# Kernel tuning notes

Measured on AMD Instinct MI355X. Metric: run time of the kernel, lower is better.

Reference implementation:

```python
import jax, jax.numpy as jnp
import numpy as np

BS, T = 128, 256
N_AGENTS, STATE_DIM, EMBED_DIM, HYPERNET_EMBED = 32, 512, 64, 256


def setup_inputs() -> dict:
    key = jax.random.key(0)
    ks = jax.random.split(key, 16)
    s = 0.02  # param init scale
    return {
        "agent_qs": jax.random.normal(ks[0], (BS, T, N_AGENTS), jnp.float32),
        "states": jax.random.normal(ks[1], (BS, T, STATE_DIM), jnp.float32),
        "w1_0": jax.random.normal(ks[2], (HYPERNET_EMBED, STATE_DIM), jnp.float32) * s,
        "b1_0": jax.random.normal(ks[3], (HYPERNET_EMBED,), jnp.float32) * s,
        "w1_2": jax.random.normal(ks[4], (EMBED_DIM * N_AGENTS, HYPERNET_EMBED), jnp.float32) * s,
        "b1_2": jax.random.normal(ks[5], (EMBED_DIM * N_AGENTS,), jnp.float32) * s,
        "wf_0": jax.random.normal(ks[6], (HYPERNET_EMBED, STATE_DIM), jnp.float32) * s,
        "bf_0": jax.random.normal(ks[7], (HYPERNET_EMBED,), jnp.float32) * s,
        "wf_2": jax.random.normal(ks[8], (EMBED_DIM, HYPERNET_EMBED), jnp.float32) * s,
        "bf_2": jax.random.normal(ks[9], (EMBED_DIM,), jnp.float32) * s,
        "hb_w": jax.random.normal(ks[10], (EMBED_DIM, STATE_DIM), jnp.float32) * s,
        "hb_b": jax.random.normal(ks[11], (EMBED_DIM,), jnp.float32) * s,
        "v0_w": jax.random.normal(ks[12], (EMBED_DIM, STATE_DIM), jnp.float32) * s,
        "v0_b": jax.random.normal(ks[13], (EMBED_DIM,), jnp.float32) * s,
        "v2_w": jax.random.normal(ks[14], (1, EMBED_DIM), jnp.float32) * s,
        "v2_b": jax.random.normal(ks[15], (1,), jnp.float32) * s,
    }


def reference(agent_qs, states, w1_0, b1_0, w1_2, b1_2, wf_0, bf_0, wf_2, bf_2,
              hb_w, hb_b, v0_w, v0_b, v2_w, v2_b):
    bs = agent_qs.shape[0]
    s = states.reshape(-1, STATE_DIM)          # [B, S]
    q = agent_qs.reshape(-1, 1, N_AGENTS)       # [B, 1, A]
    # hypernet-generated first-layer weights (positive via abs)
    h1 = jax.nn.relu(s @ w1_0.T + b1_0)
    w1 = jnp.abs(h1 @ w1_2.T + b1_2).reshape(-1, N_AGENTS, EMBED_DIM)  # [B, A, E]
    b1 = (s @ hb_w.T + hb_b).reshape(-1, 1, EMBED_DIM)                 # [B, 1, E]
    hidden = jax.nn.elu(jnp.einsum('bia,bae->bie', q, w1) + b1)        # [B, 1, E]
    # hypernet-generated final weights
    hf = jax.nn.relu(s @ wf_0.T + bf_0)
    w_final = jnp.abs(hf @ wf_2.T + bf_2).reshape(-1, EMBED_DIM, 1)    # [B, E, 1]
    v = (jax.nn.relu(s @ v0_w.T + v0_b) @ v2_w.T + v2_b).reshape(-1, 1, 1)
    y = jnp.einsum('bie,beo->bio', hidden, w_final) + v                # [B, 1, 1]
    return y.reshape(bs, -1, 1)
```

## Files before the change

### kernel.cpp

```cpp
#include <hip/hip_runtime.h>


#define SDIM 512
#define HD   256
#define EDIM 64
#define NAG  32

typedef short short8v __attribute__((ext_vector_type(8)));
typedef short short4v __attribute__((ext_vector_type(4)));
typedef float f32x4  __attribute__((ext_vector_type(4)));

__device__ __forceinline__ unsigned short f2bf(float f) {
  unsigned int u = __float_as_uint(f);
  unsigned int r = (u + 0x7FFFu + ((u >> 16) & 1u)) >> 16;
  return (unsigned short)r;
}
__device__ __forceinline__ float bf2f(unsigned short u) {
  return __uint_as_float(((unsigned int)u) << 16);
}
__device__ __forceinline__ short4v cvt4(float4 a) {
  short4v r;
  r[0] = (short)f2bf(a.x); r[1] = (short)f2bf(a.y);
  r[2] = (short)f2bf(a.z); r[3] = (short)f2bf(a.w);
  return r;
}

__global__ void qmix_convert(const float* __restrict__ w1_0, const float* __restrict__ wf_0,
                             const float* __restrict__ hb_w, const float* __restrict__ v0_w,
                             const float* __restrict__ w1_2, const float* __restrict__ wf_2,
                             unsigned short* __restrict__ W0cat, unsigned short* __restrict__ w12b,
                             unsigned short* __restrict__ wf2b) {
  int i = blockIdx.x * 256 + threadIdx.x;
  if (i < 327680) {
    float v;
    if (i < 131072)      v = w1_0[i];
    else if (i < 262144) v = wf_0[i - 131072];
    else if (i < 294912) v = hb_w[i - 262144];
    else                 v = v0_w[i - 294912];
    W0cat[i] = f2bf(v);
  } else if (i < 851968) {
    w12b[i - 327680] = f2bf(w1_2[i - 327680]);
  } else if (i < 868352) {
    wf2b[i - 851968] = f2bf(wf_2[i - 851968]);
  }
}

__global__ __launch_bounds__(512, 2) void qmix_k1(
    const float* __restrict__ states, const unsigned short* __restrict__ W0cat,
    const unsigned short* __restrict__ wf2b,
    const float* __restrict__ b1_0, const float* __restrict__ bf_0,
    const float* __restrict__ hb_b, const float* __restrict__ v0_b,
    const float* __restrict__ v2_w, const float* __restrict__ bf_2,
    unsigned short* __restrict__ h1g, unsigned short* __restrict__ b1h,
    unsigned short* __restrict__ wfinh, float* __restrict__ vbuf)
{
  __shared__ unsigned short sA[64 * 512];

  const int t    = threadIdx.x;
  const int r0   = blockIdx.x * 64;
  const int wave = t >> 6, lane = t & 63;
  const int lrow = lane & 15, lk = lane >> 4;

  const float4* gS4 = (const float4*)(states + (size_t)r0 * SDIM);
  float4 L[16];
#pragma unroll
  for (int it = 0; it < 16; it++) L[it] = gS4[it * 512 + t];

  const int colbase = wave * 80;
  const unsigned short* bp[5];
#pragma unroll
  for (int f = 0; f < 5; f++)
    bp[f] = W0cat + (size_t)(colbase + f * 16 + lrow) * SDIM + 8 * lk;
  short8v bregs[2][5];
#pragma unroll
  for (int f = 0; f < 5; f++) bregs[0][f] = *(const short8v*)(bp[f]);
#pragma unroll
  for (int f = 0; f < 5; f++) bregs[1][f] = *(const short8v*)(bp[f] + 32);

#pragma unroll
  for (int it = 0; it < 16; it++) {
    int idx = it * 512 + t;
    int row = idx >> 7, c4 = idx & 127;
    int byte = (row * 1024 + c4 * 8) ^ ((row & 7) << 4);
    *(short4v*)((char*)sA + byte) = cvt4(L[it]);
  }
  __syncthreads();

  f32x4 acc[4][5];
#pragma unroll
  for (int i = 0; i < 4; i++)
#pragma unroll
    for (int f = 0; f < 5; f++) acc[i][f] = (f32x4){0.f, 0.f, 0.f, 0.f};

#pragma unroll
  for (int ks = 0; ks < 16; ks++) {
    const int p = ks & 1;
    short8v af[4];
#pragma unroll
    for (int i = 0; i < 4; i++) {
      int row = i * 16 + lrow;
      int byte = (row * 1024 + ks * 64 + lk * 16) ^ ((row & 7) << 4);
      af[i] = *(const short8v*)((const char*)sA + byte);
    }
#pragma unroll
    for (int f = 0; f < 5; f++)
#pragma unroll
      for (int i = 0; i < 4; i++)
        acc[i][f] = __builtin_amdgcn_mfma_f32_16x16x32_bf16(af[i], bregs[p][f], acc[i][f], 0, 0, 0);
    if (ks < 14) {
#pragma unroll
      for (int f = 0; f < 5; f++) bregs[p][f] = *(const short8v*)(bp[f] + (ks + 2) * 32);
    }
  }

  __syncthreads();

  {
    float vs[4][4];
#pragma unroll
    for (int i = 0; i < 4; i++)
#pragma unroll
      for (int rr = 0; rr < 4; rr++) vs[i][rr] = 0.f;

#pragma unroll
    for (int f = 0; f < 5; f++) {
      int cb  = colbase + f * 16;
      int col = cb + lrow;
      if (cb < 512) {
        float bv = (cb < 256) ? b1_0[col] : bf_0[col - 256];
#pragma unroll
        for (int i = 0; i < 4; i++)
#pragma unroll
          for (int rr = 0; rr < 4; rr++) {
            int row = i * 16 + lk * 4 + rr;
            float v = fmaxf(acc[i][f][rr] + bv, 0.f);
            int byte = (row * 1024 + col * 2) ^ ((row & 7) << 4);
            *(unsigned short*)((char*)sA + byte) = f2bf(v);
          }
      } else if (cb < 576) {
        int e = col - 512;
        float bv = hb_b[e];
#pragma unroll
        for (int i = 0; i < 4; i++)
#pragma unroll
          for (int rr = 0; rr < 4; rr++) {
            int row = i * 16 + lk * 4 + rr;
            b1h[(size_t)(r0 + row) * EDIM + e] = f2bf(acc[i][f][rr] + bv);
          }
      } else {
        int e = col - 576;
        float bv = v0_b[e], wv = v2_w[e];
#pragma unroll
        for (int i = 0; i < 4; i++)
#pragma unroll
          for (int rr = 0; rr < 4; rr++)
            vs[i][rr] = fmaf(fmaxf(acc[i][f][rr] + bv, 0.f), wv, vs[i][rr]);
      }
    }
    if (colbase == 560) {
#pragma unroll
      for (int i = 0; i < 4; i++)
#pragma unroll
        for (int rr = 0; rr < 4; rr++) {
          float v = vs[i][rr];
#pragma unroll
          for (int m = 1; m < 16; m <<= 1) v += __shfl_xor(v, m, 64);
          if (lrow == 0) vbuf[r0 + i * 16 + lk * 4 + rr] = v;
        }
    }
  }
  __syncthreads();

  {
    const int wr2 = wave >> 1;
    const int wc2 = wave & 1;
    f32x4 wfa[2];
    wfa[0] = (f32x4){0.f, 0.f, 0.f, 0.f};
    wfa[1] = (f32x4){0.f, 0.f, 0.f, 0.f};
    const int row = wr2 * 16 + lrow;
#pragma unroll
    for (int kf = 0; kf < 8; kf++) {
      int byte = (row * 1024 + 512 + kf * 64 + lk * 16) ^ ((row & 7) << 4);
      short8v af2 = *(const short8v*)((const char*)sA + byte);
#pragma unroll
      for (int j = 0; j < 2; j++) {
        short8v bf2v = *(const short8v*)(wf2b + (size_t)(wc2 * 32 + j * 16 + lrow) * HD + kf * 32 + 8 * lk);
        wfa[j] = __builtin_amdgcn_mfma_f32_16x16x32_bf16(af2, bf2v, wfa[j], 0, 0, 0);
      }
    }
#pragma unroll
    for (int j = 0; j < 2; j++) {
      int e = wc2 * 32 + j * 16 + lrow;
#pragma unroll
      for (int r = 0; r < 4; r++) {
        int row2 = wr2 * 16 + lk * 4 + r;
        wfinh[(size_t)(r0 + row2) * EDIM + e] = f2bf(fabsf(wfa[j][r] + bf_2[e]));
      }
    }
  }

  {
    char* dst = (char*)h1g + (size_t)r0 * 512;
#pragma unroll
    for (int u = 0; u < 4; u++) {
      int idx = u * 512 + t;
      int row = idx >> 5;
      int p   = (idx & 31) * 16;
      short8v v = *(const short8v*)((const char*)sA + row * 1024 + p);
      *(short8v*)(dst + row * 512 + p) = v;
    }
  }
}

__global__ __launch_bounds__(512, 1) void qmix_k2(
    const unsigned short* __restrict__ h1g, const unsigned short* __restrict__ w12b,
    const float* __restrict__ agent_qs, const float* __restrict__ b1_2,
    const unsigned short* __restrict__ b1h, const unsigned short* __restrict__ wfinh,
    const float* __restrict__ vbuf, const float* __restrict__ v2_b,
    float* __restrict__ out)
{
  __shared__ unsigned char h1s[128 * 512];
  __shared__ unsigned short bbuf[2][16384];
  __shared__ float q_t[NAG * 136];
  __shared__ float ypart[2][128];

  const int t    = threadIdx.x;
  const int r0   = blockIdx.x * 128;
  const int wave = t >> 6, lane = t & 63;
  const int lrow = lane & 15, lk = lane >> 4;
  const int wr = wave >> 1;
  const int wc = wave & 1;

  short8v Lh[8];
  {
    const char* src = (const char*)h1g + (size_t)r0 * 512;
#pragma unroll
    for (int it = 0; it < 8; it++)
      Lh[it] = *(const short8v*)(src + (it * 512 + t) * 16);
  }
  const float4* gq = (const float4*)(agent_qs + (size_t)r0 * NAG);
  float4 q0 = gq[t], q1 = gq[512 + t];
  short8v sreg[4];
#pragma unroll
  for (int rd = 0; rd < 4; rd++)
    sreg[rd] = *(const short8v*)(w12b + rd * 4096 + t * 8);

  {
#pragma unroll
    for (int it = 0; it < 8; it++)
      *(short8v*)(h1s + (it * 512 + t) * 16) = Lh[it];
    int row0 = t >> 3, a4 = (t & 7) * 4;
    q_t[(a4 + 0) * 136 + row0] = q0.x;
    q_t[(a4 + 1) * 136 + row0] = q0.y;
    q_t[(a4 + 2) * 136 + row0] = q0.z;
    q_t[(a4 + 3) * 136 + row0] = q0.w;
    int row1 = 64 + row0;
    q_t[(a4 + 0) * 136 + row1] = q1.x;
    q_t[(a4 + 1) * 136 + row1] = q1.y;
    q_t[(a4 + 2) * 136 + row1] = q1.z;
    q_t[(a4 + 3) * 136 + row1] = q1.w;
#pragma unroll
    for (int rd = 0; rd < 4; rd++) {
      int Lo = rd * 8192 + t * 16;
      *(short8v*)((char*)bbuf + (Lo ^ (((Lo >> 9) & 7) << 4))) = sreg[rd];
    }
  }
  __syncthreads();

  short8v afr[2][8];
#pragma unroll
  for (int i = 0; i < 2; i++) {
    int row = wr * 32 + i * 16 + lrow;
#pragma unroll
    for (int kf = 0; kf < 8; kf++)
      afr[i][kf] = *(const short8v*)(h1s + row * 512 + ((kf * 64 + lk * 16) ^ ((row & 7) << 4)));
  }

  f32x4 hac00 = (f32x4){0.f,0.f,0.f,0.f}, hac01 = (f32x4){0.f,0.f,0.f,0.f};
  f32x4 hac10 = (f32x4){0.f,0.f,0.f,0.f}, hac11 = (f32x4){0.f,0.f,0.f,0.f};

#pragma unroll 1
  for (int a = 0; a < NAG; a++) {
    if (a < NAG - 1) {
      const unsigned short* p = w12b + (size_t)(a + 1) * 16384;
#pragma unroll
      for (int rd = 0; rd < 4; rd++)
        sreg[rd] = *(const short8v*)(p + rd * 4096 + t * 8);
    }
    const char* rbase = (const char*)bbuf + (a & 1) * 32768;

    f32x4 T00 = (f32x4){0.f,0.f,0.f,0.f}, T01 = (f32x4){0.f,0.f,0.f,0.f};
    f32x4 T10 = (f32x4){0.f,0.f,0.f,0.f}, T11 = (f32x4){0.f,0.f,0.f,0.f};
    const int e0 = wc * 32 + lrow, e1 = e0 + 16;
#pragma unroll
    for (int kf = 0; kf < 8; kf++) {
      short8v b0  = *(const short8v*)(rbase + ((e0 * 512 + kf * 64 + lk * 16) ^ ((e0 & 7) << 4)));
      short8v b1v = *(const short8v*)(rbase + ((e1 * 512 + kf * 64 + lk * 16) ^ ((e1 & 7) << 4)));
      T00 = __builtin_amdgcn_mfma_f32_16x16x32_bf16(afr[0][kf], b0,  T00, 0, 0, 0);
      T10 = __builtin_amdgcn_mfma_f32_16x16x32_bf16(afr[1][kf], b0,  T10, 0, 0, 0);
      T01 = __builtin_amdgcn_mfma_f32_16x16x32_bf16(afr[0][kf], b1v, T01, 0, 0, 0);
      T11 = __builtin_amdgcn_mfma_f32_16x16x32_bf16(afr[1][kf], b1v, T11, 0, 0, 0);
    }
    float bb0 = b1_2[a * EDIM + e0];
    float bb1 = b1_2[a * EDIM + e1];
    float4 qa = *(const float4*)(&q_t[a * 136 + wr * 32 + lk * 4]);
    float4 qb = *(const float4*)(&q_t[a * 136 + wr * 32 + 16 + lk * 4]);
#pragma unroll
    for (int r = 0; r < 4; r++) {
      float qar = (r == 0) ? qa.x : (r == 1) ? qa.y : (r == 2) ? qa.z : qa.w;
      float qbr = (r == 0) ? qb.x : (r == 1) ? qb.y : (r == 2) ? qb.z : qb.w;
      hac00[r] = fmaf(qar, fabsf(T00[r] + bb0), hac00[r]);
      hac01[r] = fmaf(qar, fabsf(T01[r] + bb1), hac01[r]);
      hac10[r] = fmaf(qbr, fabsf(T10[r] + bb0), hac10[r]);
      hac11[r] = fmaf(qbr, fabsf(T11[r] + bb1), hac11[r]);
    }
    if (a < NAG - 1) {
      char* wb = (char*)bbuf + ((a & 1) ^ 1) * 32768;
#pragma unroll
      for (int rd = 0; rd < 4; rd++) {
        int Lo = rd * 8192 + t * 16;
        *(short8v*)(wb + (Lo ^ (((Lo >> 9) & 7) << 4))) = sreg[rd];
      }
    }
    __syncthreads();
  }

  {
    float ys0[4], ys1[4];
    const int e0 = wc * 32 + lrow, e1 = e0 + 16;
#pragma unroll
    for (int r = 0; r < 4; r++) {
      int row0 = wr * 32 + lk * 4 + r;
      int row1 = row0 + 16;
      size_t g0 = (size_t)(r0 + row0) * EDIM;
      size_t g1 = (size_t)(r0 + row1) * EDIM;
      float p00 = hac00[r] + bf2f(b1h[g0 + e0]);
      float p01 = hac01[r] + bf2f(b1h[g0 + e1]);
      float p10 = hac10[r] + bf2f(b1h[g1 + e0]);
      float p11 = hac11[r] + bf2f(b1h[g1 + e1]);
      float h00 = p00 > 0.f ? p00 : expm1f(p00);
      float h01 = p01 > 0.f ? p01 : expm1f(p01);
      float h10 = p10 > 0.f ? p10 : expm1f(p10);
      float h11 = p11 > 0.f ? p11 : expm1f(p11);
      ys0[r] = h00 * bf2f(wfinh[g0 + e0]) + h01 * bf2f(wfinh[g0 + e1]);
      ys1[r] = h10 * bf2f(wfinh[g1 + e0]) + h11 * bf2f(wfinh[g1 + e1]);
    }
#pragma unroll
    for (int m = 1; m < 16; m <<= 1)
#pragma unroll
      for (int r = 0; r < 4; r++) {
        ys0[r] += __shfl_xor(ys0[r], m, 64);
        ys1[r] += __shfl_xor(ys1[r], m, 64);
      }
    if (lrow == 0) {
#pragma unroll
      for (int r = 0; r < 4; r++) {
        ypart[wc][wr * 32 + lk * 4 + r]      = ys0[r];
        ypart[wc][wr * 32 + 16 + lk * 4 + r] = ys1[r];
      }
    }
  }
  __syncthreads();
  if (t < 128) {
    out[r0 + t] = ypart[0][t] + ypart[1][t] + vbuf[r0 + t] + v2_b[0];
  }
}

extern "C" void kernel_launch(void* const* d_in, const int* in_sizes, int n_in,
                              void* d_out, int out_size, void* d_ws, size_t ws_size,
                              hipStream_t stream) {
  const float* agent_qs = (const float*)d_in[0];
  const float* states   = (const float*)d_in[1];
  const float* w1_0 = (const float*)d_in[2];
  const float* b1_0 = (const float*)d_in[3];
  const float* w1_2 = (const float*)d_in[4];
  const float* b1_2 = (const float*)d_in[5];
  const float* wf_0 = (const float*)d_in[6];
  const float* bf_0 = (const float*)d_in[7];
  const float* wf_2 = (const float*)d_in[8];
  const float* bf_2 = (const float*)d_in[9];
  const float* hb_w = (const float*)d_in[10];
  const float* hb_b = (const float*)d_in[11];
  const float* v0_w = (const float*)d_in[12];
  const float* v0_b = (const float*)d_in[13];
  const float* v2_w = (const float*)d_in[14];
  const float* v2_b = (const float*)d_in[15];

  char* ws = (char*)d_ws;
  unsigned short* W0cat = (unsigned short*)ws;
  unsigned short* w12b  = (unsigned short*)(ws + 655360);
  unsigned short* wf2b  = (unsigned short*)(ws + 1703936);
  unsigned short* h1g   = (unsigned short*)(ws + 1736704);
  unsigned short* b1h   = (unsigned short*)(ws + 18513920);
  unsigned short* wfinh = (unsigned short*)(ws + 22708224);
  float*          vbuf  = (float*)(ws + 26902528);

  qmix_convert<<<3392, 256, 0, stream>>>(w1_0, wf_0, hb_w, v0_w, w1_2, wf_2,
                                         W0cat, w12b, wf2b);
  qmix_k1<<<512, 512, 0, stream>>>(states, W0cat, wf2b, b1_0, bf_0, hb_b, v0_b,
                                   v2_w, bf_2, h1g, b1h, wfinh, vbuf);
  qmix_k2<<<256, 512, 0, stream>>>(h1g, w12b, agent_qs, b1_2, b1h, wfinh, vbuf,
                                   v2_b, (float*)d_out);
}
```

Baseline: 113.7 us.

## Stage hypernet weight tiles in double-buffered LDS and retile waves 2x4

The first GEMM in qmix_k1 no longer has each wave load its own B-fragments straight from global memory. The block now cooperatively loads 32-wide K slices of the concatenated weight matrix into a double-buffered, swizzled LDS buffer, with a barrier per K step. Waves are rearranged into 2 row groups by 4 column chunks, each computing 32 rows by 160 columns, so every B fragment feeds two MFMAs. This cuts redundant global weight traffic but adds about 80KB of LDS, drops occupancy to one block per CU, and puts 16 barriers in the main loop.

After: 106.5 us. 1.07x faster.

```diff
diff --git a/kernel.cpp b/kernel.cpp
--- a/kernel.cpp
+++ b/kernel.cpp
@@ -45,7 +45,7 @@
   }
 }
 
-__global__ __launch_bounds__(512, 2) void qmix_k1(
+__global__ __launch_bounds__(512, 1) void qmix_k1(
     const float* __restrict__ states, const unsigned short* __restrict__ W0cat,
     const unsigned short* __restrict__ wf2b,
     const float* __restrict__ b1_0, const float* __restrict__ bf_0,
@@ -55,27 +55,28 @@
     unsigned short* __restrict__ wfinh, float* __restrict__ vbuf)
 {
   __shared__ unsigned short sA[64 * 512];
+  __shared__ unsigned short bbuf[2][20480];
 
   const int t    = threadIdx.x;
   const int r0   = blockIdx.x * 64;
   const int wave = t >> 6, lane = t & 63;
   const int lrow = lane & 15, lk = lane >> 4;
+  const int rg = wave >> 2;
+  const int ch = wave & 3;
+  const int colbase = ch * 160;
 
   const float4* gS4 = (const float4*)(states + (size_t)r0 * SDIM);
   float4 L[16];
 #pragma unroll
   for (int it = 0; it < 16; it++) L[it] = gS4[it * 512 + t];
 
-  const int colbase = wave * 80;
-  const unsigned short* bp[5];
-#pragma unroll
-  for (int f = 0; f < 5; f++)
-    bp[f] = W0cat + (size_t)(colbase + f * 16 + lrow) * SDIM + 8 * lk;
-  short8v bregs[2][5];
-#pragma unroll
-  for (int f = 0; f < 5; f++) bregs[0][f] = *(const short8v*)(bp[f]);
-#pragma unroll
-  for (int f = 0; f < 5; f++) bregs[1][f] = *(const short8v*)(bp[f] + 32);
+  short8v breg[5];
+#pragma unroll
+  for (int j = 0; j < 5; j++) {
+    int m = j * 512 + t;
+    int col = m >> 2, kslot = m & 3;
+    breg[j] = *(const short8v*)(W0cat + (size_t)col * SDIM + kslot * 8);
+  }
 
 #pragma unroll
   for (int it = 0; it < 16; it++) {
@@ -84,56 +85,76 @@
     int byte = (row * 1024 + c4 * 8) ^ ((row & 7) << 4);
     *(short4v*)((char*)sA + byte) = cvt4(L[it]);
   }
+#pragma unroll
+  for (int j = 0; j < 5; j++) {
+    int m = j * 512 + t;
+    int col = m >> 2, kslot = m & 3;
+    *(short8v*)((char*)bbuf + col * 64 + ((kslot * 16) ^ ((col & 3) << 4))) = breg[j];
+  }
   __syncthreads();
 
-  f32x4 acc[4][5];
-#pragma unroll
-  for (int i = 0; i < 4; i++)
-#pragma unroll
-    for (int f = 0; f < 5; f++) acc[i][f] = (f32x4){0.f, 0.f, 0.f, 0.f};
-
-#pragma unroll
+  f32x4 acc[2][10];
+#pragma unroll
+  for (int i = 0; i < 2; i++)
+#pragma unroll
+    for (int f = 0; f < 10; f++) acc[i][f] = (f32x4){0.f, 0.f, 0.f, 0.f};
+
+#pragma unroll 1
   for (int ks = 0; ks < 16; ks++) {
-    const int p = ks & 1;
-    short8v af[4];
-#pragma unroll
-    for (int i = 0; i < 4; i++) {
-      int row = i * 16 + lrow;
-      int byte = (row * 1024 + ks * 64 + lk * 16) ^ ((row & 7) << 4);
-      af[i] = *(const short8v*)((const char*)sA + byte);
-    }
-#pragma unroll
-    for (int f = 0; f < 5; f++)
-#pragma unroll
-      for (int i = 0; i < 4; i++)
-        acc[i][f] = __builtin_amdgcn_mfma_f32_16x16x32_bf16(af[i], bregs[p][f], acc[i][f], 0, 0, 0);
-    if (ks < 14) {
-#pragma unroll
-      for (int f = 0; f < 5; f++) bregs[p][f] = *(const short8v*)(bp[f] + (ks + 2) * 32);
-    }
-  }
-
-  __syncthreads();
-
-  {
-    float vs[4][4];
-#pragma unroll
-    for (int i = 0; i < 4; i++)
+    if (ks < 15) {
+#pragma unroll
+      for (int j = 0; j < 5; j++) {
+        int m = j * 512 + t;
+        int col = m >> 2, kslot = m & 3;
+        breg[j] = *(const short8v*)(W0cat + (size_t)col * SDIM + (ks + 1) * 32 + kslot * 8);
+      }
+    }
+    const char* rb = (const char*)bbuf + (ks & 1) * 40960;
+    short8v af0, af1;
+    {
+      int row = rg * 32 + lrow;
+      af0 = *(const short8v*)((const char*)sA + ((row * 1024 + ks * 64 + lk * 16) ^ ((row & 7) << 4)));
+      row = rg * 32 + 16 + lrow;
+      af1 = *(const short8v*)((const char*)sA + ((row * 1024 + ks * 64 + lk * 16) ^ ((row & 7) << 4)));
+    }
+#pragma unroll
+    for (int cf = 0; cf < 10; cf++) {
+      int col = colbase + cf * 16 + lrow;
+      short8v b = *(const short8v*)(rb + col * 64 + ((lk * 16) ^ ((col & 3) << 4)));
+      acc[0][cf] = __builtin_amdgcn_mfma_f32_16x16x32_bf16(af0, b, acc[0][cf], 0, 0, 0);
+      acc[1][cf] = __builtin_amdgcn_mfma_f32_16x16x32_bf16(af1, b, acc[1][cf], 0, 0, 0);
+    }
+    if (ks < 15) {
+      char* wb = (char*)bbuf + ((ks + 1) & 1) * 40960;
+#pragma unroll
+      for (int j = 0; j < 5; j++) {
+        int m = j * 512 + t;
+        int col = m >> 2, kslot = m & 3;
+        *(short8v*)(wb + col * 64 + ((kslot * 16) ^ ((col & 3) << 4))) = breg[j];
+      }
+    }
+    __syncthreads();
+  }
+
+  {
+    float vs[2][4];
+#pragma unroll
+    for (int i = 0; i < 2; i++)
 #pragma unroll
       for (int rr = 0; rr < 4; rr++) vs[i][rr] = 0.f;
 
 #pragma unroll
-    for (int f = 0; f < 5; f++) {
-      int cb  = colbase + f * 16;
+    for (int cf = 0; cf < 10; cf++) {
+      int cb  = colbase + cf * 16;
       int col = cb + lrow;
       if (cb < 512) {
         float bv = (cb < 256) ? b1_0[col] : bf_0[col - 256];
 #pragma unroll
-        for (int i = 0; i < 4; i++)
+        for (int i = 0; i < 2; i++)
 #pragma unroll
           for (int rr = 0; rr < 4; rr++) {
-            int row = i * 16 + lk * 4 + rr;
-            float v = fmaxf(acc[i][f][rr] + bv, 0.f);
+            int row = rg * 32 + i * 16 + lk * 4 + rr;
+            float v = fmaxf(acc[i][cf][rr] + bv, 0.f);
             int byte = (row * 1024 + col * 2) ^ ((row & 7) << 4);
             *(unsigned short*)((char*)sA + byte) = f2bf(v);
           }
@@ -141,31 +162,31 @@
         int e = col - 512;
         float bv = hb_b[e];
 #pragma unroll
-        for (int i = 0; i < 4; i++)
+        for (int i = 0; i < 2; i++)
 #pragma unroll
           for (int rr = 0; rr < 4; rr++) {
-            int row = i * 16 + lk * 4 + rr;
-            b1h[(size_t)(r0 + row) * EDIM + e] = f2bf(acc[i][f][rr] + bv);
+            int row = rg * 32 + i * 16 + lk * 4 + rr;
+            b1h[(size_t)(r0 + row) * EDIM + e] = f2bf(acc[i][cf][rr] + bv);
           }
       } else {
         int e = col - 576;
         float bv = v0_b[e], wv = v2_w[e];
 #pragma unroll
-        for (int i = 0; i < 4; i++)
+        for (int i = 0; i < 2; i++)
 #pragma unroll
           for (int rr = 0; rr < 4; rr++)
-            vs[i][rr] = fmaf(fmaxf(acc[i][f][rr] + bv, 0.f), wv, vs[i][rr]);
-      }
-    }
-    if (colbase == 560) {
-#pragma unroll
-      for (int i = 0; i < 4; i++)
+            vs[i][rr] = fmaf(fmaxf(acc[i][cf][rr] + bv, 0.f), wv, vs[i][rr]);
+      }
+    }
+    if (ch == 3) {
+#pragma unroll
+      for (int i = 0; i < 2; i++)
 #pragma unroll
         for (int rr = 0; rr < 4; rr++) {
           float v = vs[i][rr];
 #pragma unroll
           for (int m = 1; m < 16; m <<= 1) v += __shfl_xor(v, m, 64);
-          if (lrow == 0) vbuf[r0 + i * 16 + lk * 4 + rr] = v;
+          if (lrow == 0) vbuf[r0 + rg * 32 + i * 16 + lk * 4 + rr] = v;
         }
     }
   }
```
